# Kernel tuning notes

Hardware: AMD Instinct MI355X
Metric: run time of the kernel (lower is better)

Reference implementation:

```python
import jax, jax.numpy as jnp
import numpy as np

N_NODES = 100000
N_CLASSES = 16
N_UEDGES = 1600000
ITERATIONS = 4
EPS = 1e-12
BETA = 3.0


def setup_inputs() -> dict:
    key = jax.random.key(0)
    k1, k2, k3 = jax.random.split(key, 3)
    # undirected edge endpoints
    s0 = jax.random.randint(k1, (N_UEDGES,), 0, N_NODES)
    d0 = jax.random.randint(k2, (N_UEDGES,), 0, N_NODES)
    # directed edges: e carries message src[e] -> dst[e]; rev[e] is the opposite direction
    src = jnp.concatenate([s0, d0])
    dst = jnp.concatenate([d0, s0])
    ar = jnp.arange(N_UEDGES)
    rev = jnp.concatenate([ar + N_UEDGES, ar])
    # prior: positive, row-normalized (labeled nodes would be peaked; generic positive prior)
    u = jax.random.uniform(k3, (N_NODES, N_CLASSES), minval=0.05, maxval=1.0, dtype=jnp.float32)
    prior = u / jnp.maximum(u.sum(-1, keepdims=True), EPS)
    # log edge potential: log(beta) on the diagonal, 0 off-diagonal (as in __init__)
    log_psi = jnp.log(jnp.float32(BETA)) * jnp.eye(N_CLASSES, dtype=jnp.float32)
    return {"prior": prior, "log_psi": log_psi, "src": src, "dst": dst,
            "rev": rev, "iterations": ITERATIONS}


def reference(prior, log_psi, src, dst, rev, iterations):
    n, k = prior.shape
    psi = jnp.exp(log_psi)  # [k,k]
    e2 = src.shape[0]
    # all messages start uniform (non-edge entries in the original [n,n,k] tensor are never read)
    m = jnp.full((e2, k), 1.0 / k, dtype=prior.dtype)

    def step(m, _):
        log_m = jnp.log(m)
        # S[i] = sum of log incoming messages to node i (product in log-space)
        S = jax.ops.segment_sum(log_m, dst, num_segments=n)  # [n,k]
        # leave-one-out: product over nbrs of src[e] excluding dst[e] == exclude reverse message
        loo = jnp.exp(S[src] - log_m[rev])  # [E2,k]
        b = jnp.maximum(prior[src] * loo, EPS)
        m_new = b @ psi
        m_new = m_new / jnp.maximum(m_new.sum(-1, keepdims=True), EPS)
        return m_new, None

    m, _ = jax.lax.scan(step, m, None, length=int(iterations))

    # beliefs: prior * product of all incoming messages, normalized per node
    S = jax.ops.segment_sum(jnp.log(m), dst, num_segments=n)
    b = jnp.maximum(prior * jnp.exp(S), EPS)
    return b / jnp.maximum(b.sum(-1, keepdims=True), EPS)
```

## Files before the change

kernel.cpp:

```cpp
#include <hip/hip_runtime.h>
#include <math.h>


#define KC 16
#define EPSF 1e-12f
#define LOG_EPS (-27.631021115928547f)
#define BLOCK 256
#define LMU (-2.7725887222397811f)
#define RANGE_BITS 15
#define RANGE (1 << RANGE_BITS)
#define HW8 (RANGE / 4)
#define BPR 64
#define ECAP 4096
#define GRID1 1024

struct Args {
  const float* prior;
  const float* log_psi;
  const int* src;
  const int* dst;
  unsigned int* histos;
  int* deg;
  float* corr;
  int* gcnt;
  int* elist;
  float* out;
  int n, nk, e2, nr;
};

__device__ __forceinline__ void psi_consts(const float* __restrict__ log_psi,
                                           float* __restrict__ cm1, float& thr) {
#pragma unroll
  for (int c = 0; c < KC; c++) cm1[c] = __expf(log_psi[c * (KC + 1)]) - 1.0f;
  float cmax = cm1[0], cmin = cm1[0];
#pragma unroll
  for (int c = 1; c < KC; c++) { cmax = fmaxf(cmax, cm1[c]); cmin = fminf(cmin, cm1[c]); }
  thr = (cmin >= 0.f && cmax == cmin) ? (LOG_EPS - __logf(16.f + cmax) - 1e-3f)
                                      : -3.0e38f;
}

__device__ __forceinline__ void g_h(const float* __restrict__ Ta,
                                    const float* __restrict__ prev,
                                    const float* __restrict__ cm1,
                                    float* __restrict__ out) {
  float b[KC], t = 0.f;
#pragma unroll
  for (int c = 0; c < KC; c++) {
    float e = fmaxf(__expf(Ta[c] - prev[c]), EPSF);
    b[c] = e; t += e;
  }
  float vs = 0.f;
#pragma unroll
  for (int c = 0; c < KC; c++) {
    float v = fmaf(cm1[c], b[c], t);
    out[c] = v; vs += v;
  }
  float ls = __logf(fmaxf(vs, EPSF));
#pragma unroll
  for (int c = 0; c < KC; c++) out[c] = __logf(out[c]) - ls;
}

template <int S>
__device__ bool msg_rec(int a, int b, const Args& A, const float* __restrict__ cm1,
                        float thr, int ds, float* __restrict__ out) {
  int dgi = A.deg[a];
  if (dgi > ds) {
#pragma unroll
    for (int c = 0; c < KC; c++) out[c] = LMU;
    return false;
  }
  float Ta[KC];
  const float* pr = A.prior + (size_t)a * KC;
  float dg = (float)dgi;
  float mx = -3.0e38f;
  if constexpr (S >= 2) {
    const float* co = A.corr + (size_t)(S - 2) * A.nk + (size_t)a * KC;
#pragma unroll
    for (int c = 0; c < KC; c++) {
      float t = fmaf(LMU, dg, __logf(pr[c])) + co[c];
      Ta[c] = t; mx = fmaxf(mx, t);
    }
  } else {
#pragma unroll
    for (int c = 0; c < KC; c++) {
      float t = fmaf(LMU, dg, __logf(pr[c]));
      Ta[c] = t; mx = fmaxf(mx, t);
    }
  }
  if (mx < thr) {
#pragma unroll
    for (int c = 0; c < KC; c++) out[c] = LMU;
    return false;
  }
  float prev[KC];
  if constexpr (S == 1) {
#pragma unroll
    for (int c = 0; c < KC; c++) prev[c] = LMU;
  } else {
    msg_rec<S - 1>(b, a, A, cm1, thr, ds, prev);
  }
  g_h(Ta, prev, cm1, out);
  return true;
}

__global__ void __launch_bounds__(BLOCK) hist_kernel(Args A) {
  __shared__ unsigned int h[HW8];
  const int tid = threadIdx.x, job = blockIdx.x;
  const int r = job >> 6, bi = job & (BPR - 1);
  for (int k = tid; k < HW8; k += BLOCK) h[k] = 0u;
  __syncthreads();
  const int lo = r << RANGE_BITS;
  const int nv = A.e2 >> 2;
  const int4* d4 = (const int4*)A.dst;
  for (int v = bi * BLOCK + tid; v < nv; v += BPR * BLOCK) {
    int4 x = d4[v];
    int a;
    a = x.x - lo; if ((unsigned)a < RANGE) atomicAdd(&h[a >> 2], 1u << ((a & 3) << 3));
    a = x.y - lo; if ((unsigned)a < RANGE) atomicAdd(&h[a >> 2], 1u << ((a & 3) << 3));
    a = x.z - lo; if ((unsigned)a < RANGE) atomicAdd(&h[a >> 2], 1u << ((a & 3) << 3));
    a = x.w - lo; if ((unsigned)a < RANGE) atomicAdd(&h[a >> 2], 1u << ((a & 3) << 3));
  }
  if (bi == 0) {
    for (int e = (nv << 2) + tid; e < A.e2; e += BLOCK) {
      int a = A.dst[e] - lo;
      if ((unsigned)a < RANGE) atomicAdd(&h[a >> 2], 1u << ((a & 3) << 3));
    }
  }
  __syncthreads();
  unsigned int* o = A.histos + (size_t)job * HW8;
  for (int k = tid; k < HW8; k += BLOCK) o[k] = h[k];

  if (job == 0 && tid == 0) {
    float cm1[KC], thr2;
    psi_consts(A.log_psi, cm1, thr2);
    float cmax = cm1[0], cmin = cm1[0];
#pragma unroll
    for (int c = 1; c < KC; c++) { cmax = fmaxf(cmax, cm1[c]); cmin = fminf(cmin, cm1[c]); }
    int ds = 0x7fffffff, dsb = 0x7fffffff;
    if (cmin >= 0.f && cmax == cmin) {
      float t = LOG_EPS - __logf(16.f + cmax) - 1e-3f;
      float denom = LMU + log1pf(cmax);
      if (denom < 0.f) {
        ds  = (int)floorf(t / denom);
        dsb = (int)floorf((LOG_EPS - 1e-3f) / denom) + 1;
      }
    }
    A.gcnt[0] = 0;
    A.gcnt[1] = ds;
    A.gcnt[2] = dsb;
  }
}

__global__ void __launch_bounds__(BLOCK) deg_kernel(Args A) {
  int i = blockIdx.x * BLOCK + threadIdx.x;
  if (i >= A.n) return;
  int r = i >> RANGE_BITS, local = i & (RANGE - 1);
  int word = local >> 2, sh = (local & 3) << 3;
  const unsigned int* base = A.histos + ((size_t)r * BPR) * HW8 + word;
  unsigned int s = 0;
#pragma unroll 4
  for (int k = 0; k < BPR; k++) s += (base[(size_t)k * HW8] >> sh) & 0xffu;
  A.deg[i] = (int)s;
  if ((int)s <= A.gcnt[1]) {
    float4 z; z.x = 0.f; z.y = 0.f; z.z = 0.f; z.w = 0.f;
#pragma unroll
    for (int g = 0; g < 4; g++) {
      float4* c4 = (float4*)(A.corr + (size_t)g * A.nk + (size_t)i * KC);
      c4[0] = z; c4[1] = z; c4[2] = z; c4[3] = z;
    }
  }
}

__global__ void __launch_bounds__(BLOCK) gen1_compact(Args A, int chunk) {
  __shared__ int ebuf[ECAP];
  __shared__ int cnt_s, base_s;
  const int tid = threadIdx.x;
  float cm1[KC], thr;
  psi_consts(A.log_psi, cm1, thr);
  const int ds = A.gcnt[1];
  const int e0 = blockIdx.x * chunk;
  const int e1 = min(e0 + chunk, A.e2);
  for (int s0 = e0; s0 < e1; s0 += ECAP) {
    int s1 = min(s0 + ECAP, e1);
    if (tid == 0) cnt_s = 0;
    __syncthreads();
    for (int e = s0 + tid; e < s1; e += BLOCK) {
      if (A.deg[A.src[e]] <= ds) { int p = atomicAdd(&cnt_s, 1); ebuf[p] = e; }
    }
    __syncthreads();
    if (tid == 0) base_s = atomicAdd(A.gcnt, cnt_s);
    __syncthreads();
    const int cs = cnt_s, bs = base_s;
    for (int k = tid; k < cs; k += BLOCK) {
      int e = ebuf[k];
      A.elist[bs + k] = e;
      int j = A.src[e], i = A.dst[e];
      float m[KC];
      if (!msg_rec<1>(j, i, A, cm1, thr, ds, m)) continue;
      float* cp = A.corr + (size_t)i * KC;
#pragma unroll
      for (int c = 0; c < KC; c++) unsafeAtomicAdd(cp + c, m[c] - LMU);
    }
    __syncthreads();
  }
}

template <int GEN>
__global__ void __launch_bounds__(BLOCK) gen_kernel(Args A) {
  float cm1[KC], thr;
  psi_consts(A.log_psi, cm1, thr);
  float* corrG = A.corr + (size_t)(GEN - 1) * A.nk;
  const int ds = A.gcnt[1];
  const int cnt = A.gcnt[0];
  const int stride = (int)gridDim.x * BLOCK;
  for (int k = blockIdx.x * BLOCK + threadIdx.x; k < cnt; k += stride) {
    int e = A.elist[k];
    int j = A.src[e], i = A.dst[e];
    float m[KC];
    if (!msg_rec<GEN>(j, i, A, cm1, thr, ds, m)) continue;
    float* cp = corrG + (size_t)i * KC;
#pragma unroll
    for (int c = 0; c < KC; c++) unsafeAtomicAdd(cp + c, m[c] - LMU);
  }
}

__global__ void __launch_bounds__(BLOCK) belief_kernel(Args A) {
  int t = blockIdx.x * BLOCK + threadIdx.x;
  if (t >= A.n * 4) return;
  int i = t >> 2;
  int dg = A.deg[i];
  float4* o4 = (float4*)A.out;
  if (dg >= A.gcnt[2]) {
    float4 u; u.x = 0.0625f; u.y = 0.0625f; u.z = 0.0625f; u.w = 0.0625f;
    o4[t] = u;
    return;
  }
  const float* corr4 = A.corr + 3 * (size_t)A.nk;
  float4 p = ((const float4*)A.prior)[t];
  float4 co = ((const float4*)corr4)[t];
  float ddg = (float)dg;
  float4 v;
  v.x = fmaxf(__expf(fmaf(LMU, ddg, __logf(p.x)) + co.x), EPSF);
  v.y = fmaxf(__expf(fmaf(LMU, ddg, __logf(p.y)) + co.y), EPSF);
  v.z = fmaxf(__expf(fmaf(LMU, ddg, __logf(p.z)) + co.z), EPSF);
  v.w = fmaxf(__expf(fmaf(LMU, ddg, __logf(p.w)) + co.w), EPSF);
  float s = (v.x + v.y) + (v.z + v.w);
  s += __shfl_xor(s, 1);
  s += __shfl_xor(s, 2);
  s = fmaxf(s, EPSF);
  float4 o;
  o.x = v.x / s; o.y = v.y / s; o.z = v.z / s; o.w = v.w / s;
  o4[t] = o;
}

extern "C" void kernel_launch(void* const* d_in, const int* in_sizes, int n_in,
                              void* d_out, int out_size, void* d_ws, size_t ws_size,
                              hipStream_t stream) {
  Args A;
  A.prior   = (const float*)d_in[0];
  A.log_psi = (const float*)d_in[1];
  A.src     = (const int*)d_in[2];
  A.dst     = (const int*)d_in[3];

  int e2 = in_sizes[2];
  int n  = in_sizes[0] / KC;
  A.n = n; A.nk = n * KC; A.e2 = e2;
  A.nr = (n + RANGE - 1) >> RANGE_BITS;

  char* ws = (char*)d_ws;
  size_t off = 0;
  auto alloc = [&](size_t bytes) -> void* {
    void* p = ws + off;
    off = (off + bytes + 255) & ~(size_t)255;
    return p;
  };
  A.histos = (unsigned int*)alloc((size_t)A.nr * BPR * HW8 * 4);
  A.deg    = (int*)alloc((size_t)n * sizeof(int));
  A.corr   = (float*)alloc((size_t)4 * A.nk * sizeof(float));
  A.gcnt   = (int*)alloc(256);
  A.elist  = (int*)alloc((size_t)e2 * sizeof(int));
  A.out    = (float*)d_out;

  const int gHist = A.nr * BPR;
  const int gDeg  = (n + BLOCK - 1) / BLOCK;
  const int chunk = (e2 + GRID1 - 1) / GRID1;
  const int gBel  = (n * 4 + BLOCK - 1) / BLOCK;

  hist_kernel<<<gHist, BLOCK, 0, stream>>>(A);
  deg_kernel<<<gDeg, BLOCK, 0, stream>>>(A);
  gen1_compact<<<GRID1, BLOCK, 0, stream>>>(A, chunk);
  gen_kernel<2><<<128, BLOCK, 0, stream>>>(A);
  gen_kernel<3><<<128, BLOCK, 0, stream>>>(A);
  gen_kernel<4><<<128, BLOCK, 0, stream>>>(A);
  belief_kernel<<<gBel, BLOCK, 0, stream>>>(A);
}
```

Measured before the change: 157.2 us.

## Compact active-active edges via bitmask and run all generations in one block

The degree kernel now writes a per-node activity bitmask using wave ballots. A new compaction kernel reads src/dst as int4, tests both endpoints against the bitmask held in LDS, and keeps only edges whose endpoints are both low-degree. The four message generations, which were one fused compaction+gen1 kernel plus three 128-block kernels, now run inside a single one-block kernel separated by fences and barriers, with corr read through relaxed atomic loads. This removes launches and shrinks the edge list, but it relies on the active edge count staying small enough for one block to process serially.

```diff
diff --git a/kernel.cpp b/kernel.cpp
--- a/kernel.cpp
+++ b/kernel.cpp
@@ -11,8 +11,7 @@
 #define RANGE (1 << RANGE_BITS)
 #define HW8 (RANGE / 4)
 #define BPR 64
-#define ECAP 4096
-#define GRID1 1024
+#define MW_LDS 4096
 
 struct Args {
   const float* prior;
@@ -23,6 +22,7 @@
   int* deg;
   float* corr;
   int* gcnt;
+  unsigned int* actmask;
   int* elist;
   float* out;
   int n, nk, e2, nr;
@@ -74,10 +74,11 @@
   float dg = (float)dgi;
   float mx = -3.0e38f;
   if constexpr (S >= 2) {
-    const float* co = A.corr + (size_t)(S - 2) * A.nk + (size_t)a * KC;
+    float* co = A.corr + (size_t)(S - 2) * A.nk + (size_t)a * KC;
 #pragma unroll
     for (int c = 0; c < KC; c++) {
-      float t = fmaf(LMU, dg, __logf(pr[c])) + co[c];
+      float cv = __hip_atomic_load(co + c, __ATOMIC_RELAXED, __HIP_MEMORY_SCOPE_AGENT);
+      float t = fmaf(LMU, dg, __logf(pr[c])) + cv;
       Ta[c] = t; mx = fmaxf(mx, t);
     }
   } else {
@@ -153,15 +154,26 @@
 
 __global__ void __launch_bounds__(BLOCK) deg_kernel(Args A) {
   int i = blockIdx.x * BLOCK + threadIdx.x;
-  if (i >= A.n) return;
-  int r = i >> RANGE_BITS, local = i & (RANGE - 1);
-  int word = local >> 2, sh = (local & 3) << 3;
-  const unsigned int* base = A.histos + ((size_t)r * BPR) * HW8 + word;
-  unsigned int s = 0;
+  bool valid = i < A.n;
+  int s = 0;
+  if (valid) {
+    int r = i >> RANGE_BITS, local = i & (RANGE - 1);
+    int word = local >> 2, sh = (local & 3) << 3;
+    const unsigned int* base = A.histos + ((size_t)r * BPR) * HW8 + word;
+    unsigned int u = 0;
 #pragma unroll 4
-  for (int k = 0; k < BPR; k++) s += (base[(size_t)k * HW8] >> sh) & 0xffu;
-  A.deg[i] = (int)s;
-  if ((int)s <= A.gcnt[1]) {
+    for (int k = 0; k < BPR; k++) u += (base[(size_t)k * HW8] >> sh) & 0xffu;
+    s = (int)u;
+    A.deg[i] = s;
+  }
+  bool act = valid && (s <= A.gcnt[1]);
+  unsigned long long b = __ballot(act);
+  if ((threadIdx.x & 63) == 0) {
+    int w = i >> 5;
+    A.actmask[w]     = (unsigned int)b;
+    A.actmask[w + 1] = (unsigned int)(b >> 32);
+  }
+  if (act) {
     float4 z; z.x = 0.f; z.y = 0.f; z.z = 0.f; z.w = 0.f;
 #pragma unroll
     for (int g = 0; g < 4; g++) {
@@ -171,49 +183,48 @@
   }
 }
 
-__global__ void __launch_bounds__(BLOCK) gen1_compact(Args A, int chunk) {
-  __shared__ int ebuf[ECAP];
-  __shared__ int cnt_s, base_s;
+__device__ __forceinline__ bool bit_on(const unsigned int* m, int i) {
+  return (m[(unsigned)i >> 5] >> (i & 31)) & 1u;
+}
+
+__global__ void __launch_bounds__(BLOCK) compactAA(Args A) {
+  __shared__ unsigned int mask[MW_LDS];
   const int tid = threadIdx.x;
-  float cm1[KC], thr;
-  psi_consts(A.log_psi, cm1, thr);
-  const int ds = A.gcnt[1];
-  const int e0 = blockIdx.x * chunk;
-  const int e1 = min(e0 + chunk, A.e2);
-  for (int s0 = e0; s0 < e1; s0 += ECAP) {
-    int s1 = min(s0 + ECAP, e1);
-    if (tid == 0) cnt_s = 0;
+  const int nw = (A.n + 31) >> 5;
+  const unsigned int* mp;
+  if (nw <= MW_LDS) {
+    for (int k = tid; k < nw; k += BLOCK) mask[k] = A.actmask[k];
     __syncthreads();
-    for (int e = s0 + tid; e < s1; e += BLOCK) {
-      if (A.deg[A.src[e]] <= ds) { int p = atomicAdd(&cnt_s, 1); ebuf[p] = e; }
-    }
-    __syncthreads();
-    if (tid == 0) base_s = atomicAdd(A.gcnt, cnt_s);
-    __syncthreads();
-    const int cs = cnt_s, bs = base_s;
-    for (int k = tid; k < cs; k += BLOCK) {
-      int e = ebuf[k];
-      A.elist[bs + k] = e;
-      int j = A.src[e], i = A.dst[e];
-      float m[KC];
-      if (!msg_rec<1>(j, i, A, cm1, thr, ds, m)) continue;
-      float* cp = A.corr + (size_t)i * KC;
-#pragma unroll
-      for (int c = 0; c < KC; c++) unsafeAtomicAdd(cp + c, m[c] - LMU);
-    }
-    __syncthreads();
+    mp = mask;
+  } else {
+    mp = A.actmask;
+  }
+  const int nv = A.e2 >> 2;
+  const int4* s4 = (const int4*)A.src;
+  const int4* d4 = (const int4*)A.dst;
+  const int stride = (int)gridDim.x * BLOCK;
+  for (int v = blockIdx.x * BLOCK + tid; v < nv; v += stride) {
+    int4 s = s4[v], d = d4[v];
+    int e = v << 2;
+    if (bit_on(mp, s.x) && bit_on(mp, d.x)) { int p = atomicAdd(A.gcnt, 1); A.elist[p] = e; }
+    if (bit_on(mp, s.y) && bit_on(mp, d.y)) { int p = atomicAdd(A.gcnt, 1); A.elist[p] = e + 1; }
+    if (bit_on(mp, s.z) && bit_on(mp, d.z)) { int p = atomicAdd(A.gcnt, 1); A.elist[p] = e + 2; }
+    if (bit_on(mp, s.w) && bit_on(mp, d.w)) { int p = atomicAdd(A.gcnt, 1); A.elist[p] = e + 3; }
+  }
+  if (blockIdx.x == 0) {
+    for (int e = (nv << 2) + tid; e < A.e2; e += BLOCK) {
+      if (bit_on(mp, A.src[e]) && bit_on(mp, A.dst[e])) {
+        int p = atomicAdd(A.gcnt, 1); A.elist[p] = e;
+      }
+    }
   }
 }
 
 template <int GEN>
-__global__ void __launch_bounds__(BLOCK) gen_kernel(Args A) {
-  float cm1[KC], thr;
-  psi_consts(A.log_psi, cm1, thr);
+__device__ __forceinline__ void gen_pass(const Args& A, const float* __restrict__ cm1,
+                                         float thr, int ds, int cnt) {
   float* corrG = A.corr + (size_t)(GEN - 1) * A.nk;
-  const int ds = A.gcnt[1];
-  const int cnt = A.gcnt[0];
-  const int stride = (int)gridDim.x * BLOCK;
-  for (int k = blockIdx.x * BLOCK + threadIdx.x; k < cnt; k += stride) {
+  for (int k = threadIdx.x; k < cnt; k += BLOCK) {
     int e = A.elist[k];
     int j = A.src[e], i = A.dst[e];
     float m[KC];
@@ -222,6 +233,20 @@
 #pragma unroll
     for (int c = 0; c < KC; c++) unsafeAtomicAdd(cp + c, m[c] - LMU);
   }
+}
+
+__global__ void __launch_bounds__(BLOCK) gens_kernel(Args A) {
+  float cm1[KC], thr;
+  psi_consts(A.log_psi, cm1, thr);
+  const int ds  = A.gcnt[1];
+  const int cnt = A.gcnt[0];
+  gen_pass<1>(A, cm1, thr, ds, cnt);
+  __threadfence(); __syncthreads();
+  gen_pass<2>(A, cm1, thr, ds, cnt);
+  __threadfence(); __syncthreads();
+  gen_pass<3>(A, cm1, thr, ds, cnt);
+  __threadfence(); __syncthreads();
+  gen_pass<4>(A, cm1, thr, ds, cnt);
 }
 
 __global__ void __launch_bounds__(BLOCK) belief_kernel(Args A) {
@@ -274,23 +299,21 @@
     off = (off + bytes + 255) & ~(size_t)255;
     return p;
   };
-  A.histos = (unsigned int*)alloc((size_t)A.nr * BPR * HW8 * 4);
-  A.deg    = (int*)alloc((size_t)n * sizeof(int));
-  A.corr   = (float*)alloc((size_t)4 * A.nk * sizeof(float));
-  A.gcnt   = (int*)alloc(256);
-  A.elist  = (int*)alloc((size_t)e2 * sizeof(int));
-  A.out    = (float*)d_out;
+  A.histos  = (unsigned int*)alloc((size_t)A.nr * BPR * HW8 * 4);
+  A.deg     = (int*)alloc((size_t)n * sizeof(int));
+  A.corr    = (float*)alloc((size_t)4 * A.nk * sizeof(float));
+  A.gcnt    = (int*)alloc(256);
+  A.actmask = (unsigned int*)alloc((((size_t)n + 31) / 32 + 128) * 4);
+  A.elist   = (int*)alloc((size_t)e2 * sizeof(int));
+  A.out     = (float*)d_out;
 
   const int gHist = A.nr * BPR;
   const int gDeg  = (n + BLOCK - 1) / BLOCK;
-  const int chunk = (e2 + GRID1 - 1) / GRID1;
   const int gBel  = (n * 4 + BLOCK - 1) / BLOCK;
 
   hist_kernel<<<gHist, BLOCK, 0, stream>>>(A);
   deg_kernel<<<gDeg, BLOCK, 0, stream>>>(A);
-  gen1_compact<<<GRID1, BLOCK, 0, stream>>>(A, chunk);
-  gen_kernel<2><<<128, BLOCK, 0, stream>>>(A);
-  gen_kernel<3><<<128, BLOCK, 0, stream>>>(A);
-  gen_kernel<4><<<128, BLOCK, 0, stream>>>(A);
+  compactAA<<<512, BLOCK, 0, stream>>>(A);
+  gens_kernel<<<1, BLOCK, 0, stream>>>(A);
   belief_kernel<<<gBel, BLOCK, 0, stream>>>(A);
 }
```

Measured after the change: 134.4 us. 1.17x faster.
